# Kernel optimization log

Measured on AMD Instinct MI355X. Metric: run time of the kernel, lower is better.

The kernel has to match this reference:

```python
import jax, jax.numpy as jnp
import numpy as np

B, N = 16, 2048
EMB_DIM = 512
K = 20          # neighbor_num
S = 1           # support_num

def _norm(x, axis):
    # F.normalize: x / max(||x||, 1e-12)
    return x / jnp.maximum(jnp.linalg.norm(x, axis=axis, keepdims=True), 1e-12)

def knn(verts, k):
    # verts: (b, v, 3); squared-distance knn excluding self
    inner = jnp.einsum('bvd,bwd->bvw', verts, verts)
    quad = jnp.sum(verts * verts, axis=2)
    dist = quad[:, :, None] - 2.0 * inner + quad[:, None, :]
    _, idx = jax.lax.top_k(-dist, k + 1)
    return idx[:, :, 1:]

def gather_nb(x, idx):
    # x: (b, v, c), idx: (b, v, n) -> (b, v, n, c)
    return jax.vmap(lambda t, i: t[i])(x, idx)

def dir_norm(verts, idx):
    d = gather_nb(verts, idx) - verts[:, :, None, :]
    return _norm(d, -1)

def conv_surface(idx, verts, directions, kernel_num):
    theta = jax.nn.relu(jnp.einsum('bvnd,dk->bvnk', dir_norm(verts, idx), _norm(directions, 0)))
    b, v, n, _ = theta.shape
    theta = theta.reshape(b, v, n, S, kernel_num)
    return jnp.sum(jnp.max(theta, axis=2), axis=2)  # (b, v, kernel_num)

def conv_layer(idx, verts, fm, w, bias, directions, out_ch):
    theta = jax.nn.relu(jnp.einsum('bvnd,dk->bvnk', dir_norm(verts, idx), _norm(directions, 0)))
    feat = fm @ w + bias                            # (b, v, (S+1)*out_ch)
    center = feat[:, :, :out_ch]
    support = gather_nb(feat[:, :, out_ch:], idx)   # (b, v, n, S*out_ch)
    b, v, n, _ = support.shape
    act = (theta * support).reshape(b, v, n, S, out_ch)
    return center + jnp.sum(jnp.max(act, axis=2), axis=2)

def pool_layer(verts, fm, key, pooling_rate=4, neighbor_num=4):
    b, v, _ = verts.shape
    idx = knn(verts, neighbor_num)
    pooled = jnp.max(gather_nb(fm, idx), axis=2)
    samp = jax.random.permutation(key, v)[: v // pooling_rate]
    return verts[:, samp, :], pooled[:, samp, :]

def _forward(xyz, w1, b1, w2, b2, w3, b3, w4, b4, fcw, fcb, dir0,
             wc1, bc1, dir1, wc2, bc2, dir2, wc3, bc3, dir3, wc4, bc4, dir4,
             clw1, clb1, bn_gamma, bn_beta, clw2, clb2):
    relu = jax.nn.relu
    # PointNet trunk (Conv1d with kernel 1 == per-point matmul)
    x = relu(jnp.einsum('oc,bcn->bon', w1, xyz) + b1[None, :, None])
    x = relu(jnp.einsum('oc,bcn->bon', w2, x) + b2[None, :, None])
    gf = jnp.max(x, axis=2, keepdims=True)
    x = jnp.concatenate([x, jnp.broadcast_to(gf, x.shape)], axis=1)
    x = relu(jnp.einsum('oc,bcn->bon', w3, x) + b3[None, :, None])
    x = relu(jnp.einsum('oc,bcn->bon', w4, x) + b4[None, :, None])
    x = jnp.max(x, axis=2)                          # (B, 1024)
    # GCN3D trunk
    verts = jnp.transpose(xyz, (0, 2, 1))           # (B, N, 3)
    idx = knn(verts, K)
    fm0 = relu(conv_surface(idx, verts, dir0, 32))
    fm1 = relu(conv_layer(idx, verts, fm0, wc1, bc1, dir1, 64))
    verts, fm1 = pool_layer(verts, fm1, jax.random.key(1))
    idx = knn(verts, K)
    fm2 = relu(conv_layer(idx, verts, fm1, wc2, bc2, dir2, 128))
    fm3 = relu(conv_layer(idx, verts, fm2, wc3, bc3, dir3, 256))
    verts, fm3 = pool_layer(verts, fm3, jax.random.key(2))
    idx = knn(verts, K)
    fm4 = conv_layer(idx, verts, fm3, wc4, bc4, dir4, 1024)
    fg = jnp.max(fm4, axis=1)                       # (B, 1024)
    fc_data = jnp.concatenate([x, fg], axis=1)      # (B, 2048)
    embedding = fc_data @ fcw.T + fcb
    # classifier, eval mode: Dropout -> identity; BN uses running mean 0 / var 1
    h = fc_data @ clw1.T + clb1
    h = relu(h / jnp.sqrt(1.0 + 1e-5) * bn_gamma + bn_beta)
    pred = h @ clw2.T + clb2
    return embedding, pred

def setup_inputs():
    key = jax.random.key(0)
    ks = jax.random.split(key, 32)
    rn = lambda k, shp: jax.random.normal(k, shp, dtype=jnp.float32) * 0.05
    return {
        'xyz': jax.random.normal(ks[0], (B, 3, N), dtype=jnp.float32),
        'w1': rn(ks[1], (64, 3)), 'b1': rn(ks[2], (64,)),
        'w2': rn(ks[3], (128, 64)), 'b2': rn(ks[4], (128,)),
        'w3': rn(ks[5], (256, 256)), 'b3': rn(ks[6], (256,)),
        'w4': rn(ks[7], (1024, 256)), 'b4': rn(ks[8], (1024,)),
        'fcw': rn(ks[9], (EMB_DIM, 2048)), 'fcb': rn(ks[10], (EMB_DIM,)),
        'dir0': rn(ks[11], (3, 32)),
        'wc1': rn(ks[12], (32, 128)), 'bc1': rn(ks[13], (128,)), 'dir1': rn(ks[14], (3, 64)),
        'wc2': rn(ks[15], (64, 256)), 'bc2': rn(ks[16], (256,)), 'dir2': rn(ks[17], (3, 128)),
        'wc3': rn(ks[18], (128, 512)), 'bc3': rn(ks[19], (512,)), 'dir3': rn(ks[20], (3, 256)),
        'wc4': rn(ks[21], (256, 2048)), 'bc4': rn(ks[22], (2048,)), 'dir4': rn(ks[23], (3, 1024)),
        'clw1': rn(ks[24], (512, 2048)), 'clb1': rn(ks[25], (512,)),
        'bn_gamma': jnp.ones((512,), dtype=jnp.float32),
        'bn_beta': jnp.zeros((512,), dtype=jnp.float32),
        'clw2': rn(ks[26], (6, 512)), 'clb2': rn(ks[27], (6,)),
    }

def reference(xyz, w1, b1, w2, b2, w3, b3, w4, b4, fcw, fcb, dir0, wc1, bc1, dir1, wc2, bc2, dir2, wc3, bc3, dir3, wc4, bc4, dir4, clw1, clb1, bn_gamma, bn_beta, clw2, clb2):
    return _forward(xyz, w1, b1, w2, b2, w3, b3, w4, b4, fcw, fcb, dir0, wc1, bc1, dir1, wc2, bc2, dir2, wc3, bc3, dir3, wc4, bc4, dir4, clw1, clb1, bn_gamma, bn_beta, clw2, clb2)
```

## Files before the change

kernel.cpp:

```cpp
#include <hip/hip_runtime.h>
#include <hip/hip_bf16.h>
#include <math.h>

#define BB 16
#define NN 2048

typedef __attribute__((ext_vector_type(8))) short s8v;
typedef __attribute__((ext_vector_type(4))) float f4v;

__global__ void k_sentinel(float* o, int n, float v){
  int i = blockIdx.x*256 + threadIdx.x;
  if (i < n) o[i] = v;
}

__device__ __forceinline__ ushort f2bf(float x){
  unsigned u = __float_as_uint(x);
  unsigned r = u + 0x7FFFu + ((u>>16)&1u);
  return (ushort)(r>>16);
}
__device__ __forceinline__ void splitbf(float v, ushort &h, ushort &l){
  h = f2bf(v);
  float hf = __uint_as_float((unsigned)h<<16);
  l = f2bf(v-hf);
}


__global__ void k_wsrm(const float* __restrict__ src, ushort* __restrict__ dh,
                       ushort* __restrict__ dl, int total){
  int id = blockIdx.x*256 + threadIdx.x;
  if (id >= total) return;
  ushort h,l; splitbf(src[id], h, l);
  dh[id]=h; dl[id]=l;
}

__global__ void k_wstr(const float* __restrict__ src, ushort* __restrict__ dh,
                       ushort* __restrict__ dl, int K, int C){
  int id = blockIdx.x*256 + threadIdx.x;
  if (id >= K*C) return;
  int c = id % C, k = id / C;
  ushort h,l; splitbf(src[id], h, l);
  dh[(size_t)c*K + k]=h; dl[(size_t)c*K + k]=l;
}


__global__ void k_mlp1s(const float* __restrict__ xyz, const float* __restrict__ w1,
                        const float* __restrict__ b1, ushort* __restrict__ xh,
                        ushort* __restrict__ xl){
  int id = blockIdx.x*256 + threadIdx.x;
  if (id >= BB*NN*64) return;
  int o = id & 63, n = (id>>6) & (NN-1), b = id>>17;
  float acc = b1[o];
  #pragma unroll
  for (int c=0;c<3;c++)
    acc += w1[o*3+c] * xyz[(size_t)(b*3+c)*NN + n];
  acc = fmaxf(acc, 0.f);
  ushort h,l; splitbf(acc, h, l);
  xh[id]=h; xl[id]=l;
}

__global__ __launch_bounds__(256) void k_rowmax(const float* __restrict__ x, float* __restrict__ o,
                                                ushort* __restrict__ gh, ushort* __restrict__ gl, int cols){
  __shared__ float sm[256];
  int row = blockIdx.x, t = threadIdx.x;
  const float* xr = x + (size_t)row*cols;
  float m = -INFINITY;
  for (int c=t;c<cols;c+=256) m = fmaxf(m, xr[c]);
  sm[t]=m; __syncthreads();
  for (int s=128;s>0;s>>=1){ if (t<s) sm[t]=fmaxf(sm[t], sm[t+s]); __syncthreads(); }
  if (!t){
    o[row]=sm[0];
    ushort h,l; splitbf(sm[0], h, l);
    gh[row]=h; gl[row]=l;
  }
}

template<int EPI, int RELU, int BCOL>
__global__ __launch_bounds__(256) void k_bgemm(
    const ushort* __restrict__ Ahg, const ushort* __restrict__ Alg,
    const ushort* __restrict__ Bhg, const ushort* __restrict__ Blg,
    const ushort* __restrict__ gfh, const ushort* __restrict__ gfl,
    const float* __restrict__ bias,
    float* __restrict__ outp, float* __restrict__ pmaxp,
    ushort* __restrict__ oth, ushort* __restrict__ otl,
    int K, int ksplit, int Kb, int N, size_t sBT, size_t sOut, int M)
{
  __shared__ ushort Ah[128][40], Al[128][40];
  __shared__ ushort Bh[64][40],  Bl[64][40];
  __shared__ float red[2][128];
  int t = threadIdx.x, z = blockIdx.z;
  int o0 = blockIdx.y*128, n0 = blockIdx.x*64;
  int wid = t>>6, lane = t&63;
  int wm = wid>>1, wn = wid&1;
  int lr = lane&15, kg = lane>>4;

  f4v acc[4][2];
  #pragma unroll
  for (int i=0;i<4;i++)
    #pragma unroll
    for (int j=0;j<2;j++) acc[i][j] = (f4v){0.f,0.f,0.f,0.f};

  for (int k0=0; k0<K; k0+=32){
    __syncthreads();
    #pragma unroll
    for (int i=0;i<2;i++){
      int j = i*256+t, oo = j>>2, k8 = (j&3)*8;
      size_t sp = (size_t)(o0+oo)*K + k0 + k8;
      *(s8v*)&Ah[oo][k8] = *(const s8v*)(Ahg+sp);
      *(s8v*)&Al[oo][k8] = *(const s8v*)(Alg+sp);
    }
    {
      int nn = t>>2, k8 = (t&3)*8, gk = k0+k8;
      const ushort *sh, *sl;
      if (gk < ksplit){
        size_t sp = (size_t)z*sBT + (size_t)(n0+nn)*Kb + gk;
        sh = Bhg+sp; sl = Blg+sp;
      } else {
        size_t sp = (size_t)z*(K-ksplit) + (gk-ksplit);
        sh = gfh+sp; sl = gfl+sp;
      }
      *(s8v*)&Bh[nn][k8] = *(const s8v*)sh;
      *(s8v*)&Bl[nn][k8] = *(const s8v*)sl;
    }
    __syncthreads();

    s8v ah[4], al[4], bh[2], bl[2];
    #pragma unroll
    for (int mt=0;mt<4;mt++){
      int row = wm*64 + mt*16 + lr;
      ah[mt] = *(const s8v*)&Ah[row][kg*8];
      al[mt] = *(const s8v*)&Al[row][kg*8];
    }
    #pragma unroll
    for (int nt=0;nt<2;nt++){
      int col = wn*32 + nt*16 + lr;
      bh[nt] = *(const s8v*)&Bh[col][kg*8];
      bl[nt] = *(const s8v*)&Bl[col][kg*8];
    }
    #pragma unroll
    for (int mt=0;mt<4;mt++)
      #pragma unroll
      for (int nt=0;nt<2;nt++){
        acc[mt][nt] = __builtin_amdgcn_mfma_f32_16x16x32_bf16(ah[mt], bh[nt], acc[mt][nt], 0,0,0);
        acc[mt][nt] = __builtin_amdgcn_mfma_f32_16x16x32_bf16(ah[mt], bl[nt], acc[mt][nt], 0,0,0);
        acc[mt][nt] = __builtin_amdgcn_mfma_f32_16x16x32_bf16(al[mt], bh[nt], acc[mt][nt], 0,0,0);
      }
  }

  if (EPI == 1){
    #pragma unroll
    for (int mt=0;mt<4;mt++){
      #pragma unroll
      for (int e=0;e<4;e++){
        int row = o0 + wm*64 + mt*16 + kg*4 + e;
        float bv = bias[row];
        float m = fmaxf(fmaxf(acc[mt][0][e]+bv, 0.f), fmaxf(acc[mt][1][e]+bv, 0.f));
        m = fmaxf(m, __shfl_xor(m, 1, 64));
        m = fmaxf(m, __shfl_xor(m, 2, 64));
        m = fmaxf(m, __shfl_xor(m, 4, 64));
        m = fmaxf(m, __shfl_xor(m, 8, 64));
        if (lr == 0) red[wn][wm*64 + mt*16 + kg*4 + e] = m;
      }
    }
    __syncthreads();
    if (t < 128){
      float m = fmaxf(red[0][t], red[1][t]);
      pmaxp[((size_t)z*M + o0 + t)*gridDim.x + blockIdx.x] = m;
    }
  } else {
    #pragma unroll
    for (int mt=0;mt<4;mt++){
      #pragma unroll
      for (int nt=0;nt<2;nt++){
        int col = n0 + wn*32 + nt*16 + lr;
        #pragma unroll
        for (int e=0;e<4;e++){
          int row = o0 + wm*64 + mt*16 + kg*4 + e;
          float bv = BCOL ? bias[col] : bias[row];
          float v = acc[mt][nt][e] + bv;
          if (RELU) v = fmaxf(v, 0.f);
          if (EPI == 0 || EPI == 2)
            outp[(size_t)z*sOut + (size_t)row*N + col] = v;
          if (EPI >= 2){
            ushort h,l; splitbf(v, h, l);
            size_t p = ((size_t)z*N + col)*(size_t)M + row;
            oth[p]=h; otl[p]=l;
          }
        }
      }
    }
  }
}

__global__ void k_xmax(const float* __restrict__ pmax, float* __restrict__ xmax){
  int id = blockIdx.x*256 + threadIdx.x;
  if (id >= BB*1024) return;
  float m = pmax[(size_t)id*32];
  for (int k=1;k<32;k++) m = fmaxf(m, pmax[(size_t)id*32+k]);
  xmax[id] = m;
}


#define TF2BODY \
  unsigned ks2 = 0x1BD11BDAu ^ k0 ^ k1; \
  unsigned a = x0 + k0, b = x1 + k1; \
  { \
  a += b; b = (b<<13)|(b>>19); b ^= a; \
  a += b; b = (b<<15)|(b>>17); b ^= a; \
  a += b; b = (b<<26)|(b>>6);  b ^= a; \
  a += b; b = (b<<6) |(b>>26); b ^= a;  a += k1;  b += ks2 + 1u; \
  a += b; b = (b<<17)|(b>>15); b ^= a; \
  a += b; b = (b<<29)|(b>>3);  b ^= a; \
  a += b; b = (b<<16)|(b>>16); b ^= a; \
  a += b; b = (b<<24)|(b>>8);  b ^= a;  a += ks2; b += k0  + 2u; \
  a += b; b = (b<<13)|(b>>19); b ^= a; \
  a += b; b = (b<<15)|(b>>17); b ^= a; \
  a += b; b = (b<<26)|(b>>6);  b ^= a; \
  a += b; b = (b<<6) |(b>>26); b ^= a;  a += k0;  b += k1  + 3u; \
  a += b; b = (b<<17)|(b>>15); b ^= a; \
  a += b; b = (b<<29)|(b>>3);  b ^= a; \
  a += b; b = (b<<16)|(b>>16); b ^= a; \
  a += b; b = (b<<24)|(b>>8);  b ^= a;  a += k1;  b += ks2 + 4u; \
  a += b; b = (b<<13)|(b>>19); b ^= a; \
  a += b; b = (b<<15)|(b>>17); b ^= a; \
  a += b; b = (b<<26)|(b>>6);  b ^= a; \
  a += b; b = (b<<6) |(b>>26); b ^= a;  a += ks2; b += k0  + 5u; \
  } \
  o0 = a; o1 = b;

__device__ __forceinline__ void tf2(unsigned k0, unsigned k1, unsigned x0, unsigned x1,
                                    unsigned &o0, unsigned &o1){ TF2BODY }
static void tf2h(unsigned k0, unsigned k1, unsigned x0, unsigned x1,
                 unsigned &o0, unsigned &o1){ TF2BODY }

__global__ void k_permkeys(int n, unsigned sk0, unsigned sk1, unsigned* __restrict__ keys){
  int i = blockIdx.x*256 + threadIdx.x;
  if (i < n){ unsigned a,b2; tf2(sk0, sk1, 0u, (unsigned)i, a, b2); keys[i] = a ^ b2; }
}

__global__ void k_permrank(int n, const unsigned* __restrict__ keys,
                           const int* __restrict__ vin, int* __restrict__ vout){
  int i = blockIdx.x*256 + threadIdx.x;
  if (i >= n) return;
  unsigned ki = keys[i];
  int rank = 0;
  for (int j=0;j<n;j++){
    unsigned kj = keys[j];
    rank += (kj < ki) || (kj == ki && j < i);
  }
  vout[rank] = vin ? vin[i] : i;
}


__global__ void k_transpose(const float* __restrict__ xyz, float* __restrict__ verts){
  int id = blockIdx.x*256 + threadIdx.x;
  if (id >= BB*NN*3) return;
  int c = id % 3, v = (id/3) % NN, b = id/(3*NN);
  verts[id] = xyz[(size_t)(b*3+c)*NN + v];
}

template<int CPL, int KSEL>
__global__ __launch_bounds__(256,4) void k_knn_g(const float* __restrict__ vbcs,
                                                 const int* __restrict__ qmap, int numQ,
                                                 int* __restrict__ out){
  constexpr int V = CPL*64;
  constexpr int GS = (CPL < 8) ? CPL : 8;
  constexpr int NG = CPL/GS;
  constexpr int GSH = (GS==8)?3:((GS==4)?2:((GS==2)?1:0));
  int t = threadIdx.x, wid = t>>6, lane = t&63;
  int b = blockIdx.y;
  int q = blockIdx.x*4 + wid;
  if (q >= numQ) return;
  const float* vx = vbcs + (size_t)b*3*V;
  const float* vy = vx + V;
  const float* vz = vy + V;
  int qv = qmap ? qmap[q] : q;
  float qx = vx[qv], qy = vy[qv], qz = vz[qv];
  float qq = qx*qx + qy*qy + qz*qz;
  unsigned long long key[CPL];
  #pragma unroll
  for (int i=0;i<CPL;i++){
    int c = lane + i*64;
    float wx=vx[c], wy=vy[c], wz=vz[c];
    float inner = qx*wx + qy*wy + qz*wz;
    float ww = wx*wx + wy*wy + wz*wz;
    float d = qq - 2.f*inner + ww;
    unsigned db = __float_as_uint(d);
    db = (db & 0x80000000u) ? ~db : (db | 0x80000000u);
    key[i] = ((unsigned long long)db << 32) | (unsigned)c;
  }
  unsigned long long g[NG];
  #pragma unroll
  for (int gg=0; gg<NG; gg++){
    unsigned long long m = key[gg*GS];
    #pragma unroll
    for (int j=1;j<GS;j++){ unsigned long long kk2 = key[gg*GS+j]; m = (kk2<m)?kk2:m; }
    g[gg] = m;
  }
  unsigned long long lb = g[0];
  #pragma unroll
  for (int gg=1;gg<NG;gg++) lb = (g[gg]<lb)?g[gg]:lb;

  int* orow = out + ((size_t)b*numQ + q)*KSEL;
  unsigned long long last = 0ull;
  for (int r=0; r<=KSEL; r++){
    unsigned long long best = lb;
    #pragma unroll
    for (int off=32; off>0; off>>=1){
      unsigned long long o = __shfl_xor(best, off, 64);
      best = (o < best) ? o : best;
    }
    int c = (int)(best & 0xffffffffull);
    if (r>0 && lane==0) orow[r-1] = c;
    last = best;
    if ((c & 63) == lane){
      int gi = c >> (6 + GSH);
      #pragma unroll
      for (int gg=0; gg<NG; gg++){
        if (gg == gi){
          unsigned long long m = ~0ull;
          #pragma unroll
          for (int j=0;j<GS;j++){
            unsigned long long kk2 = key[gg*GS+j];
            unsigned long long qk = (kk2 > last) ? kk2 : ~0ull;
            m = (qk<m)?qk:m;
          }
          g[gg] = m;
        }
      }
      unsigned long long nb2 = g[0];
      #pragma unroll
      for (int gg=1;gg<NG;gg++) nb2 = (g[gg]<nb2)?g[gg]:nb2;
      lb = nb2;
    }
  }
}

__global__ void k_dirs(const float* __restrict__ verts, int V, const int* __restrict__ idx,
                       float* __restrict__ dirs, int total){
  int id = blockIdx.x*256 + threadIdx.x;
  if (id >= total) return;
  int v = (id/20) % V, b = id/(20*V);
  const float* vb = verts + (size_t)b*V*3;
  int nb = idx[id];
  float dx = vb[nb*3+0]-vb[v*3+0];
  float dy = vb[nb*3+1]-vb[v*3+1];
  float dz = vb[nb*3+2]-vb[v*3+2];
  float s = 1.f / fmaxf(sqrtf(dx*dx+dy*dy+dz*dz), 1e-12f);
  dirs[(size_t)id*3+0]=dx*s; dirs[(size_t)id*3+1]=dy*s; dirs[(size_t)id*3+2]=dz*s;
}

__global__ void k_surf(const float* __restrict__ dirs, const float* __restrict__ dir0,
                       ushort* __restrict__ fh, ushort* __restrict__ fl, int V){
  int id = blockIdx.x*256 + threadIdx.x;
  if (id >= BB*V*32) return;
  int k = id & 31; int vv = (id>>5) % V; int b = id/(32*V);
  float nx=dir0[k], ny=dir0[32+k], nz=dir0[64+k];
  float s = 1.f/fmaxf(sqrtf(nx*nx+ny*ny+nz*nz), 1e-12f);
  nx*=s; ny*=s; nz*=s;
  const float* dd = dirs + (size_t)(b*V+vv)*60;
  float m = 0.f;
  for (int n=0;n<20;n++){
    float th = dd[n*3]*nx + dd[n*3+1]*ny + dd[n*3+2]*nz;
    m = fmaxf(m, fmaxf(th, 0.f));
  }
  ushort h,l; splitbf(m, h, l);
  size_t p = (size_t)(b*V+vv)*32 + k;
  fh[p]=h; fl[p]=l;
}

template<int OUT>
__global__ void k_comb(const float* __restrict__ feat, const int* __restrict__ idx,
                       const float* __restrict__ dirs, const float* __restrict__ dw,
                       float* __restrict__ outp, ushort* __restrict__ oh, ushort* __restrict__ ol,
                       int V, int OC, int relu_flag){
  int id = blockIdx.x*256 + threadIdx.x;
  if (id >= BB*V*OC) return;
  int oc = id % OC, v = (id/OC) % V, b = id/(OC*V);
  float wx=dw[oc], wy=dw[OC+oc], wz=dw[2*OC+oc];
  float s = 1.f/fmaxf(sqrtf(wx*wx+wy*wy+wz*wz), 1e-12f);
  wx*=s; wy*=s; wz*=s;
  size_t row = (size_t)b*V + v;
  const int* ir = idx + row*20;
  const float* dd = dirs + row*60;
  float center = feat[row*2*OC + oc];
  float m = -INFINITY;
  for (int n=0;n<20;n++){
    int nb = ir[n];
    float th = dd[n*3]*wx + dd[n*3+1]*wy + dd[n*3+2]*wz;
    th = fmaxf(th, 0.f);
    float sup = feat[((size_t)b*V + nb)*2*OC + OC + oc];
    m = fmaxf(m, th*sup);
  }
  float rv = center + m;
  if (OUT == 0){
    outp[row*OC + oc] = relu_flag ? fmaxf(rv, 0.f) : rv;
  } else {
    rv = fmaxf(rv, 0.f);
    ushort h,l; splitbf(rv, h, l);
    oh[row*OC + oc]=h; ol[row*OC + oc]=l;
  }
}

template<int OUT>
__global__ void k_pool(const float* __restrict__ fm, const int* __restrict__ idx4,
                       float* __restrict__ outp, ushort* __restrict__ oh, ushort* __restrict__ ol,
                       int V, int C, int numS){
  int id = blockIdx.x*256 + threadIdx.x;
  if (id >= BB*numS*C) return;
  int c = id % C, sI = (id/C) % numS, b = id/(C*numS);
  const int* ir = idx4 + ((size_t)b*numS + sI)*4;
  float m = -INFINITY;
  for (int n=0;n<4;n++) m = fmaxf(m, fm[((size_t)b*V + ir[n])*C + c]);
  size_t p = ((size_t)b*numS + sI)*C + c;
  if (OUT == 0) outp[p] = m;
  else { ushort h,l; splitbf(m, h, l); oh[p]=h; ol[p]=l; }
}

__global__ void k_vgather(const float* __restrict__ vin, const int* __restrict__ perm,
                          float* __restrict__ vout, float* __restrict__ vbcs,
                          int V, int numS){
  int id = blockIdx.x*256 + threadIdx.x;
  if (id >= BB*numS*3) return;
  int c = id % 3, sI = (id/3) % numS, b = id/(3*numS);
  float val = vin[((size_t)b*V + perm[sI])*3 + c];
  vout[id] = val;
  vbcs[((size_t)b*3 + c)*numS + sI] = val;
}

__global__ void k_colmax(const float* __restrict__ x, float* __restrict__ o, int Vr, int C){
  int id = blockIdx.x*256 + threadIdx.x;
  if (id >= BB*C) return;
  int c = id % C, b = id / C;
  float m = -INFINITY;
  for (int v=0; v<Vr; v++) m = fmaxf(m, x[(size_t)(b*Vr+v)*C + c]);
  o[id] = m;
}


__global__ __launch_bounds__(256) void k_emb2(const float* __restrict__ xmax, const float* __restrict__ fg,
                                              const float* __restrict__ fcw, const float* __restrict__ fcb,
                                              float* __restrict__ outp){
  int gid = blockIdx.x*4 + (threadIdx.x>>6);
  int lane = threadIdx.x & 63;
  if (gid >= BB*512) return;
  int e = gid & 511, b = gid >> 9;
  const float* wr = fcw + (size_t)e*2048;
  const float* xb = xmax + b*1024;
  const float* gb = fg + b*1024;
  float acc = 0.f;
  for (int k=lane; k<1024; k+=64)
    acc += xb[k]*wr[k] + gb[k]*wr[1024+k];
  #pragma unroll
  for (int off=32; off>0; off>>=1) acc += __shfl_xor(acc, off, 64);
  if (lane==0) outp[gid] = acc + fcb[e];
}

__global__ __launch_bounds__(256) void k_h2(const float* __restrict__ xmax, const float* __restrict__ fg,
                                            const float* __restrict__ clw1, const float* __restrict__ clb1,
                                            const float* __restrict__ gamma, const float* __restrict__ beta,
                                            float* __restrict__ h){
  int gid = blockIdx.x*4 + (threadIdx.x>>6);
  int lane = threadIdx.x & 63;
  if (gid >= BB*512) return;
  int j = gid & 511, b = gid >> 9;
  const float* wr = clw1 + (size_t)j*2048;
  const float* xb = xmax + b*1024;
  const float* gb = fg + b*1024;
  float acc = 0.f;
  for (int k=lane; k<1024; k+=64)
    acc += xb[k]*wr[k] + gb[k]*wr[1024+k];
  #pragma unroll
  for (int off=32; off>0; off>>=1) acc += __shfl_xor(acc, off, 64);
  if (lane==0){
    const float inv_s = 1.0f / sqrtf(1.0f + 1e-5f);
    float v = (acc + clb1[j]) * inv_s * gamma[j] + beta[j];
    h[gid] = fmaxf(v, 0.f);
  }
}

__global__ __launch_bounds__(256) void k_pred2(const float* __restrict__ h, const float* __restrict__ clw2,
                                               const float* __restrict__ clb2, float* __restrict__ outp){
  int gid = blockIdx.x*4 + (threadIdx.x>>6);
  int lane = threadIdx.x & 63;
  if (gid >= BB*6) return;
  int o = gid % 6, b = gid / 6;
  const float* hb = h + b*512;
  const float* wr = clw2 + o*512;
  float acc = 0.f;
  for (int k=lane; k<512; k+=64) acc += hb[k]*wr[k];
  #pragma unroll
  for (int off=32; off>0; off>>=1) acc += __shfl_xor(acc, off, 64);
  if (lane==0) outp[BB*512 + gid] = acc + clb2[o];
}


static inline int cdiv(long long a, int b){ return (int)((a + b - 1)/b); }

extern "C" void kernel_launch(void* const* d_in, const int* in_sizes, int n_in,
                              void* d_out, int out_size, void* d_ws, size_t ws_size,
                              hipStream_t stream){
  float* out = (float*)d_out;
  if (n_in != 30 || in_sizes[0] != BB*3*NN || out_size != BB*512 + BB*6){
    k_sentinel<<<cdiv(out_size,256),256,0,stream>>>(out, out_size, 2000.0f);
    return;
  }
  const float* xyz  = (const float*)d_in[0];
  const float* w1   = (const float*)d_in[1];
  const float* b1   = (const float*)d_in[2];
  const float* w2   = (const float*)d_in[3];
  const float* b2   = (const float*)d_in[4];
  const float* w3   = (const float*)d_in[5];
  const float* b3   = (const float*)d_in[6];
  const float* w4   = (const float*)d_in[7];
  const float* b4   = (const float*)d_in[8];
  const float* fcw  = (const float*)d_in[9];
  const float* fcb  = (const float*)d_in[10];
  const float* dir0 = (const float*)d_in[11];
  const float* wc1  = (const float*)d_in[12];
  const float* bc1  = (const float*)d_in[13];
  const float* dir1 = (const float*)d_in[14];
  const float* wc2  = (const float*)d_in[15];
  const float* bc2  = (const float*)d_in[16];
  const float* dir2 = (const float*)d_in[17];
  const float* wc3  = (const float*)d_in[18];
  const float* bc3  = (const float*)d_in[19];
  const float* dir3 = (const float*)d_in[20];
  const float* wc4  = (const float*)d_in[21];
  const float* bc4  = (const float*)d_in[22];
  const float* dir4 = (const float*)d_in[23];
  const float* clw1 = (const float*)d_in[24];
  const float* clb1 = (const float*)d_in[25];
  const float* gma  = (const float*)d_in[26];
  const float* bta  = (const float*)d_in[27];
  const float* clw2 = (const float*)d_in[28];
  const float* clb2 = (const float*)d_in[29];

  char* w = (char*)d_ws;
  size_t off = 0;
  auto A = [&](size_t bytes){ size_t r = off; off += (bytes + 255) & ~(size_t)255; return r; };
  const size_t oXMAX = A((size_t)BB*1024*4);
  const size_t oFG   = A((size_t)BB*1024*4);
  const size_t oGF   = A((size_t)BB*128*4);
  const size_t oGFP  = A((size_t)BB*128*2*2);
  const size_t oH    = A((size_t)BB*512*4);
  const size_t oP2048= A(2048*4);
  const size_t oP512 = A(512*4);
  const size_t oPKEY = A(2048*4);
  const size_t oPA   = A(2048*4);
  const size_t oPMAX = A((size_t)BB*1024*32*4);
  const size_t oV0   = A((size_t)BB*2048*3*4);
  const size_t oV1   = A((size_t)BB*512*3*4);
  const size_t oV2   = A((size_t)BB*128*3*4);
  const size_t oV1S  = A((size_t)BB*3*512*4);
  const size_t oV2S  = A((size_t)BB*3*128*4);
  const size_t oIDX0 = A((size_t)BB*2048*20*4);
  const size_t oDIR0 = A((size_t)BB*2048*20*3*4);
  const size_t oFM0  = A((size_t)BB*2048*32*2*2);
  const size_t oFM1  = A((size_t)BB*2048*64*4);
  const size_t oI40  = A((size_t)BB*512*4*4);
  const size_t oFM1P = A((size_t)BB*512*64*2*2);
  const size_t oIDX1 = A((size_t)BB*512*20*4);
  const size_t oDIR1 = A((size_t)BB*512*20*3*4);
  const size_t oFM2  = A((size_t)BB*512*128*2*2);
  const size_t oFM3  = A((size_t)BB*512*256*4);
  const size_t oI41  = A((size_t)BB*128*4*4);
  const size_t oFM3P = A((size_t)BB*128*256*2*2);
  const size_t oIDX2 = A((size_t)BB*128*20*4);
  const size_t oDIR2 = A((size_t)BB*128*20*3*4);
  const size_t oFM4  = A((size_t)BB*128*1024*4);
  const size_t oBIGA = A((size_t)BB*256*NN*4);
  const size_t oBIGB = A((size_t)BB*128*NN*4);
  const size_t oW2P  = A((size_t)128*64*2*2);
  const size_t oW3P  = A((size_t)256*256*2*2);
  const size_t oW4P  = A((size_t)1024*256*2*2);
  const size_t oWC1T = A((size_t)32*128*2*2);
  const size_t oWC2T = A((size_t)64*256*2*2);
  const size_t oWC3T = A((size_t)128*512*2*2);
  const size_t oWC4T = A((size_t)256*2048*2*2);
  if (off > ws_size){
    k_sentinel<<<cdiv(out_size,256),256,0,stream>>>(out, out_size, 1000.0f);
    return;
  }
  float* xmax = (float*)(w+oXMAX); float* fg = (float*)(w+oFG);
  float* gf = (float*)(w+oGF);     float* hbuf = (float*)(w+oH);
  ushort* gfh = (ushort*)(w+oGFP); ushort* gfl = gfh + BB*128;
  int* p2048 = (int*)(w+oP2048);   int* p512 = (int*)(w+oP512);
  unsigned* pkeys = (unsigned*)(w+oPKEY); int* pa = (int*)(w+oPA);
  float* pmax = (float*)(w+oPMAX);
  float* v0 = (float*)(w+oV0); float* v1 = (float*)(w+oV1); float* v2 = (float*)(w+oV2);
  float* v1s = (float*)(w+oV1S); float* v2s = (float*)(w+oV2S);
  int* idx0 = (int*)(w+oIDX0); int* idx1 = (int*)(w+oIDX1); int* idx2 = (int*)(w+oIDX2);
  int* i40 = (int*)(w+oI40);   int* i41 = (int*)(w+oI41);
  float* d0 = (float*)(w+oDIR0); float* d1 = (float*)(w+oDIR1); float* d2 = (float*)(w+oDIR2);
  ushort* fm0h = (ushort*)(w+oFM0); ushort* fm0l = fm0h + (size_t)BB*2048*32;
  float* fm1 = (float*)(w+oFM1);
  ushort* fm1ph = (ushort*)(w+oFM1P); ushort* fm1pl = fm1ph + (size_t)BB*512*64;
  ushort* fm2h = (ushort*)(w+oFM2); ushort* fm2l = fm2h + (size_t)BB*512*128;
  float* fm3 = (float*)(w+oFM3);
  ushort* fm3ph = (ushort*)(w+oFM3P); ushort* fm3pl = fm3ph + (size_t)BB*128*256;
  float* fm4 = (float*)(w+oFM4);
  ushort* x1h = (ushort*)(w+oBIGA); ushort* x1l = x1h + (size_t)BB*2048*64;
  ushort* x3h = (ushort*)(w+oBIGA); ushort* x3l = x3h + (size_t)BB*2048*256;
  ushort* x2h = (ushort*)(w+oIDX0); ushort* x2l = x2h + (size_t)BB*2048*128;
  float* x2 = (float*)(w+oBIGB); float* feat = (float*)(w+oBIGB);
  ushort* w2ph = (ushort*)(w+oW2P); ushort* w2pl = w2ph + 128*64;
  ushort* w3ph = (ushort*)(w+oW3P); ushort* w3pl = w3ph + 256*256;
  ushort* w4ph = (ushort*)(w+oW4P); ushort* w4pl = w4ph + 1024*256;
  ushort* wc1h = (ushort*)(w+oWC1T); ushort* wc1l = wc1h + 32*128;
  ushort* wc2h = (ushort*)(w+oWC2T); ushort* wc2l = wc2h + 64*256;
  ushort* wc3h = (ushort*)(w+oWC3T); ushort* wc3l = wc3h + 128*512;
  ushort* wc4h = (ushort*)(w+oWC4T); ushort* wc4l = wc4h + 256*2048;

  k_wsrm<<<cdiv(128*64,256),256,0,stream>>>(w2, w2ph, w2pl, 128*64);
  k_wsrm<<<cdiv(256*256,256),256,0,stream>>>(w3, w3ph, w3pl, 256*256);
  k_wsrm<<<cdiv(1024*256,256),256,0,stream>>>(w4, w4ph, w4pl, 1024*256);
  k_wstr<<<cdiv(32*128,256),256,0,stream>>>(wc1, wc1h, wc1l, 32, 128);
  k_wstr<<<cdiv(64*256,256),256,0,stream>>>(wc2, wc2h, wc2l, 64, 256);
  k_wstr<<<cdiv(128*512,256),256,0,stream>>>(wc3, wc3h, wc3l, 128, 512);
  k_wstr<<<cdiv(256*2048,256),256,0,stream>>>(wc4, wc4h, wc4l, 256, 2048);

  k_mlp1s<<<cdiv((long long)BB*NN*64,256),256,0,stream>>>(xyz, w1, b1, x1h, x1l);
  k_bgemm<2,1,0><<<dim3(32,1,BB),256,0,stream>>>(w2ph, w2pl, x1h, x1l, nullptr, nullptr,
      b2, x2, nullptr, x2h, x2l, 64, 64, 64, 2048, (size_t)2048*64, (size_t)128*2048, 128);
  k_rowmax<<<BB*128,256,0,stream>>>(x2, gf, gfh, gfl, NN);
  k_bgemm<3,1,0><<<dim3(32,2,BB),256,0,stream>>>(w3ph, w3pl, x2h, x2l, gfh, gfl,
      b3, nullptr, nullptr, x3h, x3l, 256, 128, 128, 2048, (size_t)2048*128, 0, 256);
  k_bgemm<1,1,0><<<dim3(32,8,BB),256,0,stream>>>(w4ph, w4pl, x3h, x3l, nullptr, nullptr,
      b4, nullptr, pmax, nullptr, nullptr, 256, 256, 256, 2048, (size_t)2048*256, 0, 1024);
  k_xmax<<<cdiv(BB*1024,256),256,0,stream>>>(pmax, xmax);

  {
    unsigned ck0=0u, ck1=1u, nk0,nk1, s00,s01, s10,s11, sc0,sc1;
    tf2h(ck0,ck1, 0u,0u, nk0,nk1);
    tf2h(ck0,ck1, 0u,1u, s00,s01);
    tf2h(nk0,nk1, 0u,1u, s10,s11);
    tf2h(0u,2u,  0u,1u, sc0,sc1);
    k_permkeys<<<8,256,0,stream>>>(2048, s00, s01, pkeys);
    k_permrank<<<8,256,0,stream>>>(2048, pkeys, nullptr, pa);
    k_permkeys<<<8,256,0,stream>>>(2048, s10, s11, pkeys);
    k_permrank<<<8,256,0,stream>>>(2048, pkeys, pa, p2048);
    k_permkeys<<<2,256,0,stream>>>(512, sc0, sc1, pkeys);
    k_permrank<<<2,256,0,stream>>>(512, pkeys, nullptr, p512);
  }

  k_transpose<<<cdiv((long long)BB*NN*3,256),256,0,stream>>>(xyz, v0);
  k_knn_g<32,20><<<dim3(512,BB),256,0,stream>>>(xyz, nullptr, 2048, idx0);
  k_dirs<<<cdiv((long long)BB*2048*20,256),256,0,stream>>>(v0, 2048, idx0, d0, BB*2048*20);
  k_surf<<<cdiv((long long)BB*2048*32,256),256,0,stream>>>(d0, dir0, fm0h, fm0l, 2048);
  k_bgemm<0,0,1><<<dim3(2,256,1),256,0,stream>>>(fm0h, fm0l, wc1h, wc1l, nullptr, nullptr,
      bc1, feat, nullptr, nullptr, nullptr, 32, 32, 32, 128, 0, 0, BB*2048);
  k_comb<0><<<cdiv((long long)BB*2048*64,256),256,0,stream>>>(feat, idx0, d0, dir1, fm1, nullptr, nullptr, 2048, 64, 1);
  k_knn_g<32,4><<<dim3(128,BB),256,0,stream>>>(xyz, p2048, 512, i40);
  k_pool<1><<<cdiv((long long)BB*512*64,256),256,0,stream>>>(fm1, i40, nullptr, fm1ph, fm1pl, 2048, 64, 512);
  k_vgather<<<cdiv((long long)BB*512*3,256),256,0,stream>>>(v0, p2048, v1, v1s, 2048, 512);
  k_knn_g<8,20><<<dim3(128,BB),256,0,stream>>>(v1s, nullptr, 512, idx1);
  k_dirs<<<cdiv((long long)BB*512*20,256),256,0,stream>>>(v1, 512, idx1, d1, BB*512*20);
  k_bgemm<0,0,1><<<dim3(4,64,1),256,0,stream>>>(fm1ph, fm1pl, wc2h, wc2l, nullptr, nullptr,
      bc2, feat, nullptr, nullptr, nullptr, 64, 64, 64, 256, 0, 0, BB*512);
  k_comb<1><<<cdiv((long long)BB*512*128,256),256,0,stream>>>(feat, idx1, d1, dir2, nullptr, fm2h, fm2l, 512, 128, 1);
  k_bgemm<0,0,1><<<dim3(8,64,1),256,0,stream>>>(fm2h, fm2l, wc3h, wc3l, nullptr, nullptr,
      bc3, feat, nullptr, nullptr, nullptr, 128, 128, 128, 512, 0, 0, BB*512);
  k_comb<0><<<cdiv((long long)BB*512*256,256),256,0,stream>>>(feat, idx1, d1, dir3, fm3, nullptr, nullptr, 512, 256, 1);
  k_knn_g<8,4><<<dim3(32,BB),256,0,stream>>>(v1s, p512, 128, i41);
  k_pool<1><<<cdiv((long long)BB*128*256,256),256,0,stream>>>(fm3, i41, nullptr, fm3ph, fm3pl, 512, 256, 128);
  k_vgather<<<cdiv((long long)BB*128*3,256),256,0,stream>>>(v1, p512, v2, v2s, 512, 128);
  k_knn_g<2,20><<<dim3(32,BB),256,0,stream>>>(v2s, nullptr, 128, idx2);
  k_dirs<<<cdiv((long long)BB*128*20,256),256,0,stream>>>(v2, 128, idx2, d2, BB*128*20);
  k_bgemm<0,0,1><<<dim3(32,16,1),256,0,stream>>>(fm3ph, fm3pl, wc4h, wc4l, nullptr, nullptr,
      bc4, feat, nullptr, nullptr, nullptr, 256, 256, 256, 2048, 0, 0, BB*128);
  k_comb<0><<<cdiv((long long)BB*128*1024,256),256,0,stream>>>(feat, idx2, d2, dir4, fm4, nullptr, nullptr, 128, 1024, 0);
  k_colmax<<<cdiv(BB*1024,256),256,0,stream>>>(fm4, fg, 128, 1024);

  k_emb2<<<cdiv(BB*512,4),256,0,stream>>>(xmax, fg, fcw, fcb, out);
  k_h2<<<cdiv(BB*512,4),256,0,stream>>>(xmax, fg, clw1, clb1, gma, bta, hbuf);
  k_pred2<<<cdiv(BB*6,4),256,0,stream>>>(hbuf, clw2, clb2, out);
}
```

Baseline: 777.3 us.

## Reuse k=20 kNN results for pooling neighbors and shrink kNN key registers

The pooling layers' 4-nearest-neighbor searches are replaced by a small gather kernel that takes the first 4 entries of the already-computed 20-NN lists for the sampled points, since top-4 is a prefix of top-20 on the same vertex set. The kNN kernel now keeps 32-bit distance keys per lane and rebuilds 64-bit keys with the index on the fly, and its launch bound occupancy hint rises from 4 to 6 blocks. This removes two full kNN passes and lowers register pressure, at the cost of some extra ALU work to reconstruct keys. The reuse relies on tie-breaking being consistent between the two searches, which holds because the same key encoding is used.

```diff
diff --git a/kernel.cpp b/kernel.cpp
--- a/kernel.cpp
+++ b/kernel.cpp
@@ -259,7 +259,7 @@
 }
 
 template<int CPL, int KSEL>
-__global__ __launch_bounds__(256,4) void k_knn_g(const float* __restrict__ vbcs,
+__global__ __launch_bounds__(256,6) void k_knn_r(const float* __restrict__ vbcs,
                                                  const int* __restrict__ qmap, int numQ,
                                                  int* __restrict__ out){
   constexpr int V = CPL*64;
@@ -276,24 +276,27 @@
   int qv = qmap ? qmap[q] : q;
   float qx = vx[qv], qy = vy[qv], qz = vz[qv];
   float qq = qx*qx + qy*qy + qz*qz;
-  unsigned long long key[CPL];
+  unsigned d[CPL];
   #pragma unroll
   for (int i=0;i<CPL;i++){
     int c = lane + i*64;
     float wx=vx[c], wy=vy[c], wz=vz[c];
     float inner = qx*wx + qy*wy + qz*wz;
     float ww = wx*wx + wy*wy + wz*wz;
-    float d = qq - 2.f*inner + ww;
-    unsigned db = __float_as_uint(d);
-    db = (db & 0x80000000u) ? ~db : (db | 0x80000000u);
-    key[i] = ((unsigned long long)db << 32) | (unsigned)c;
+    float dd = qq - 2.f*inner + ww;
+    unsigned db = __float_as_uint(dd);
+    d[i] = (db & 0x80000000u) ? ~db : (db | 0x80000000u);
   }
   unsigned long long g[NG];
   #pragma unroll
   for (int gg=0; gg<NG; gg++){
-    unsigned long long m = key[gg*GS];
-    #pragma unroll
-    for (int j=1;j<GS;j++){ unsigned long long kk2 = key[gg*GS+j]; m = (kk2<m)?kk2:m; }
+    unsigned long long m = ~0ull;
+    #pragma unroll
+    for (int j=0;j<GS;j++){
+      int i = gg*GS+j;
+      unsigned long long kk = ((unsigned long long)d[i]<<32) | (unsigned)(lane + i*64);
+      m = (kk<m)?kk:m;
+    }
     g[gg] = m;
   }
   unsigned long long lb = g[0];
@@ -320,8 +323,9 @@
           unsigned long long m = ~0ull;
           #pragma unroll
           for (int j=0;j<GS;j++){
-            unsigned long long kk2 = key[gg*GS+j];
-            unsigned long long qk = (kk2 > last) ? kk2 : ~0ull;
+            int i = gg*GS+j;
+            unsigned long long kk = ((unsigned long long)d[i]<<32) | (unsigned)(lane + i*64);
+            unsigned long long qk = (kk > last) ? kk : ~0ull;
             m = (qk<m)?qk:m;
           }
           g[gg] = m;
@@ -333,6 +337,14 @@
       lb = nb2;
     }
   }
+}
+
+__global__ void k_poolidx(const int* __restrict__ idxsrc, const int* __restrict__ perm,
+                          int* __restrict__ outp, int Vsrc, int numS, int total){
+  int id = blockIdx.x*256 + threadIdx.x;
+  if (id >= total) return;
+  int j = id & 3, s = (id>>2) % numS, b = id/(numS*4);
+  outp[id] = idxsrc[((size_t)b*Vsrc + perm[s])*20 + j];
 }
 
 __global__ void k_dirs(const float* __restrict__ verts, int V, const int* __restrict__ idx,
@@ -644,16 +656,16 @@
   }
 
   k_transpose<<<cdiv((long long)BB*NN*3,256),256,0,stream>>>(xyz, v0);
-  k_knn_g<32,20><<<dim3(512,BB),256,0,stream>>>(xyz, nullptr, 2048, idx0);
+  k_knn_r<32,20><<<dim3(512,BB),256,0,stream>>>(xyz, nullptr, 2048, idx0);
   k_dirs<<<cdiv((long long)BB*2048*20,256),256,0,stream>>>(v0, 2048, idx0, d0, BB*2048*20);
   k_surf<<<cdiv((long long)BB*2048*32,256),256,0,stream>>>(d0, dir0, fm0h, fm0l, 2048);
   k_bgemm<0,0,1><<<dim3(2,256,1),256,0,stream>>>(fm0h, fm0l, wc1h, wc1l, nullptr, nullptr,
       bc1, feat, nullptr, nullptr, nullptr, 32, 32, 32, 128, 0, 0, BB*2048);
   k_comb<0><<<cdiv((long long)BB*2048*64,256),256,0,stream>>>(feat, idx0, d0, dir1, fm1, nullptr, nullptr, 2048, 64, 1);
-  k_knn_g<32,4><<<dim3(128,BB),256,0,stream>>>(xyz, p2048, 512, i40);
+  k_poolidx<<<cdiv(BB*512*4,256),256,0,stream>>>(idx0, p2048, i40, 2048, 512, BB*512*4);
   k_pool<1><<<cdiv((long long)BB*512*64,256),256,0,stream>>>(fm1, i40, nullptr, fm1ph, fm1pl, 2048, 64, 512);
   k_vgather<<<cdiv((long long)BB*512*3,256),256,0,stream>>>(v0, p2048, v1, v1s, 2048, 512);
-  k_knn_g<8,20><<<dim3(128,BB),256,0,stream>>>(v1s, nullptr, 512, idx1);
+  k_knn_r<8,20><<<dim3(128,BB),256,0,stream>>>(v1s, nullptr, 512, idx1);
   k_dirs<<<cdiv((long long)BB*512*20,256),256,0,stream>>>(v1, 512, idx1, d1, BB*512*20);
   k_bgemm<0,0,1><<<dim3(4,64,1),256,0,stream>>>(fm1ph, fm1pl, wc2h, wc2l, nullptr, nullptr,
       bc2, feat, nullptr, nullptr, nullptr, 64, 64, 64, 256, 0, 0, BB*512);
@@ -661,10 +673,10 @@
   k_bgemm<0,0,1><<<dim3(8,64,1),256,0,stream>>>(fm2h, fm2l, wc3h, wc3l, nullptr, nullptr,
       bc3, feat, nullptr, nullptr, nullptr, 128, 128, 128, 512, 0, 0, BB*512);
   k_comb<0><<<cdiv((long long)BB*512*256,256),256,0,stream>>>(feat, idx1, d1, dir3, fm3, nullptr, nullptr, 512, 256, 1);
-  k_knn_g<8,4><<<dim3(32,BB),256,0,stream>>>(v1s, p512, 128, i41);
+  k_poolidx<<<cdiv(BB*128*4,256),256,0,stream>>>(idx1, p512, i41, 512, 128, BB*128*4);
   k_pool<1><<<cdiv((long long)BB*128*256,256),256,0,stream>>>(fm3, i41, nullptr, fm3ph, fm3pl, 512, 256, 128);
   k_vgather<<<cdiv((long long)BB*128*3,256),256,0,stream>>>(v1, p512, v2, v2s, 512, 128);
-  k_knn_g<2,20><<<dim3(32,BB),256,0,stream>>>(v2s, nullptr, 128, idx2);
+  k_knn_r<2,20><<<dim3(32,BB),256,0,stream>>>(v2s, nullptr, 128, idx2);
   k_dirs<<<cdiv((long long)BB*128*20,256),256,0,stream>>>(v2, 128, idx2, d2, BB*128*20);
   k_bgemm<0,0,1><<<dim3(32,16,1),256,0,stream>>>(fm3ph, fm3pl, wc4h, wc4l, nullptr, nullptr,
       bc4, feat, nullptr, nullptr, nullptr, 256, 256, 256, 2048, 0, 0, BB*128);
```

Measured after the change: 764.0 us. No clear change (-1.7%).
